# Optimization experiments

Measured on AMD Instinct MI355X. Metric: run time of the kernel, lower is better.

## Reference

```python
import jax, jax.numpy as jnp
import numpy as np

B, N, C, M = 2, 16384, 256, 16  # M = win_w*win_h for stage 1
W = N // M

def setup_inputs() -> dict:
    key = jax.random.key(0)
    ks = jax.random.split(key, 8)
    s = 1.0 / np.sqrt(C)
    return {
        "input": jax.random.normal(ks[0], (B, N, C), jnp.float32),
        "embed_qk": jax.random.normal(ks[1], (B, W, M, M, 3), jnp.float32),
        "Wq": jax.random.normal(ks[2], (C, C), jnp.float32) * s,
        "bq": jax.random.normal(ks[3], (C,), jnp.float32) * 0.01,
        "Wk": jax.random.normal(ks[4], (C, C), jnp.float32) * s,
        "bk": jax.random.normal(ks[5], (C,), jnp.float32) * 0.01,
        "Wp": jax.random.normal(ks[6], (3, 1), jnp.float32) * 0.5,
        "bp": jax.random.normal(ks[7], (1,), jnp.float32) * 0.01,
    }

def reference(input, embed_qk, Wq, bq, Wk, bk, Wp, bp):
    WIN = 16  # stage==1 -> win_w*win_h = 4*4
    b, n, c = input.shape
    add = (-n) % WIN
    q = jax.nn.elu(input @ Wq + bq) + 1.0
    k = jax.nn.elu(input @ Wk + bk) + 1.0
    v = input
    pad = ((0, 0), (0, add), (0, 0))
    q_win = jnp.pad(q, pad).reshape(b, -1, WIN, c)
    k_win = jnp.pad(k, pad).reshape(b, -1, WIN, c)
    v_win = jnp.pad(v, pad).reshape(b, -1, WIN, c)
    # second ELU+1 feature map (as in the original)
    phi_q = jax.nn.elu(q_win) + 1.0
    phi_k = jax.nn.elu(k_win) + 1.0
    # KV sums over ALL windows w -> (b, m, c, d)
    KV = jnp.einsum('bwmc,bwmd->bmcd', phi_k, v_win)
    # (b, w, n, m, d) expanded intermediate
    att = jnp.einsum('bwnc,bmcd->bwnmd', phi_q, KV)
    p = (embed_qk @ Wp + bp)[..., 0]  # (b, w, m, m)
    att = att + p[..., None]
    out = att.reshape(b, -1, c)[:, :n, :]
    return out
```

## Files before the change

kernel.cpp:

```cpp
#include <hip/hip_runtime.h>

typedef __attribute__((ext_vector_type(8))) short s16x8;
typedef __attribute__((ext_vector_type(8))) ushort u16x8;
typedef __attribute__((ext_vector_type(4))) ushort u16x4;
typedef __attribute__((ext_vector_type(4))) float f32x4v;

namespace {

constexpr int kB = 2;
constexpr int kN = 16384;
constexpr int kC = 256;
constexpr int kQR = 1024;

__device__ __forceinline__ ushort f2bf(float f) {
  union { float f; uint u; } v; v.f = f;
  uint u = v.u + 0x7fffu + ((v.u >> 16) & 1u);
  return (ushort)(u >> 16);
}

__device__ __forceinline__ float phi_act(float x) {
  return x > 0.f ? x + 2.f : __expf(x) + 1.f;
}

__global__ __launch_bounds__(256) void wt_kernel(const float* __restrict__ Wq,
                                                 const float* __restrict__ Wk,
                                                 ushort* __restrict__ WqT,
                                                 ushort* __restrict__ WkT) {
  __shared__ float ts[64][65];
  const float* W = blockIdx.z ? Wk : Wq;
  ushort* WT = blockIdx.z ? WkT : WqT;
  const int bi = blockIdx.x, bj = blockIdx.y, t = threadIdx.x;
  for (int rep = 0; rep < 16; ++rep) {
    int e = rep * 256 + t, r = e >> 6, c = e & 63;
    ts[r][c] = W[(size_t)(bi * 64 + r) * kC + bj * 64 + c];
  }
  __syncthreads();
  for (int rep = 0; rep < 16; ++rep) {
    int e = rep * 256 + t, j = e >> 6, k = e & 63;
    WT[(size_t)(bj * 64 + j) * kC + bi * 64 + k] = f2bf(ts[k][j]);
  }
}

__global__ __launch_bounds__(256) void regroup_kernel(const float* __restrict__ X,
                                                      ushort* __restrict__ G) {
  __shared__ ushort ls[64 * 288];
  const int cb = blockIdx.x;
  const int wb = blockIdx.y;
  const int b = blockIdx.z;
  const int t = threadIdx.x;
  const float* src = X + ((size_t)b * kN + wb * 1024) * kC + cb * 16;
  const int lr = t >> 2, cg = t & 3;
  for (int rep = 0; rep < 16; ++rep) {
    int row = rep * 64 + lr;
    float4 v = *reinterpret_cast<const float4*>(src + (size_t)row * kC + cg * 4);
    int w = row >> 4, m = row & 15;
    int base = w * 288 + m * 18 + cg * 4;
    uint p0 = (uint)f2bf(v.x) | ((uint)f2bf(v.y) << 16);
    uint p1 = (uint)f2bf(v.z) | ((uint)f2bf(v.w) << 16);
    *reinterpret_cast<uint*>(ls + base) = p0;
    *reinterpret_cast<uint*>(ls + base + 2) = p1;
  }
  __syncthreads();
  const int m = t >> 4, c_l = t & 15;
  const size_t gbase = ((size_t)b * 16 + m) * 128 + wb * 8;
#pragma unroll
  for (int r = 0; r < 8; ++r) {
    u16x8 v;
#pragma unroll
    for (int wl = 0; wl < 8; ++wl) v[wl] = ls[(r * 8 + wl) * 288 + m * 18 + c_l];
    *reinterpret_cast<u16x8*>(G + (gbase + r) * 2048 + (size_t)(cb * 16 + c_l) * 8) = v;
  }
}

__global__ __launch_bounds__(512) void proj_fused(
    const float* __restrict__ X, const ushort* __restrict__ WqT,
    const ushort* __restrict__ WkT, const float* __restrict__ bq,
    const float* __restrict__ bk, ushort* __restrict__ kg,
    ushort* __restrict__ qf) {
  __shared__ __align__(16) ushort smem[24576];

  const int t = threadIdx.x, lane = t & 63, wv = t >> 6;
  const int bx = blockIdx.x;
  const bool kmode = bx < 256;
  int b, n0;
  const ushort* WT;
  const float* bias;
  if (kmode) {
    b = bx >> 7; n0 = (bx & 127) * 128; WT = WkT; bias = bk;
  } else {
    int i = bx - 256; b = i >> 3; n0 = (i & 7) * 128; WT = WqT; bias = bq;
  }
  const int wgrp = bx & 127;
  const float* Xbase = X + ((size_t)b * kN + n0) * kC;

  const int r4 = t >> 2, ca = (t & 3) << 3;
  const int bj = t >> 2, bch = t & 3;

  float4 fa0, fa1;
  u16x8 rb0, rb1;
  auto stageLoad = [&](int ks) {
    const int k0 = ks * 32;
    fa0 = *reinterpret_cast<const float4*>(Xbase + (size_t)r4 * kC + k0 + ca);
    fa1 = *reinterpret_cast<const float4*>(Xbase + (size_t)r4 * kC + k0 + ca + 4);
    rb0 = *reinterpret_cast<const u16x8*>(WT + (size_t)bj * kC + k0 + bch * 8);
    rb1 = *reinterpret_cast<const u16x8*>(WT + (size_t)(bj + 128) * kC + k0 + bch * 8);
  };
  auto stageWrite = [&](int h) {
    ushort* A = smem + h * 4096;
    ushort* B = smem + 8192 + h * 8192;
    u16x8 va;
    va[0] = f2bf(fa0.x); va[1] = f2bf(fa0.y); va[2] = f2bf(fa0.z); va[3] = f2bf(fa0.w);
    va[4] = f2bf(fa1.x); va[5] = f2bf(fa1.y); va[6] = f2bf(fa1.z); va[7] = f2bf(fa1.w);
    *reinterpret_cast<u16x8*>(A + r4 * 32 + (((t & 3) ^ ((r4 >> 1) & 3)) << 3)) = va;
    *reinterpret_cast<u16x8*>(B + bj * 32 + ((bch ^ ((bj >> 1) & 3)) << 3)) = rb0;
    *reinterpret_cast<u16x8*>(B + (bj + 128) * 32 + ((bch ^ (((bj + 128) >> 1) & 3)) << 3)) = rb1;
  };

  f32x4v acc[4][4] = {};
  const int lo = lane & 15, hi = lane >> 4;
  const int wr0 = (wv >> 2) * 64, wc0 = (wv & 3) * 64;
  auto mma = [&](int h) {
    const ushort* A = smem + h * 4096;
    const ushort* B = smem + 8192 + h * 8192;
    s16x8 af[4], bf[4];
#pragma unroll
    for (int i = 0; i < 4; ++i) {
      int r = wr0 + i * 16 + lo;
      af[i] = *reinterpret_cast<const s16x8*>(A + r * 32 + ((hi ^ ((r >> 1) & 3)) << 3));
    }
#pragma unroll
    for (int j = 0; j < 4; ++j) {
      int cj = wc0 + j * 16 + lo;
      bf[j] = *reinterpret_cast<const s16x8*>(B + cj * 32 + ((hi ^ ((cj >> 1) & 3)) << 3));
    }
#pragma unroll
    for (int i = 0; i < 4; ++i)
#pragma unroll
      for (int j = 0; j < 4; ++j)
        acc[i][j] = __builtin_amdgcn_mfma_f32_16x16x32_bf16(af[i], bf[j], acc[i][j], 0, 0, 0);
  };

  stageLoad(0);
  stageWrite(0);
  __syncthreads();
  int cur = 0;
  for (int ks = 0; ks < 8; ++ks) {
    if (ks < 7) stageLoad(ks + 1);
    __builtin_amdgcn_sched_barrier(0);
    mma(cur);
    __builtin_amdgcn_sched_barrier(0);
    if (ks < 7) stageWrite(cur ^ 1);
    __syncthreads();
    cur ^= 1;
  }

  float bv[4];
#pragma unroll
  for (int fj = 0; fj < 4; ++fj) bv[fj] = bias[wc0 + fj * 16 + lo];

  if (kmode) {
    const int m = t >> 5, cl = t & 31;
    u16x8 vout[8];
    ushort* ep = smem;
#pragma unroll
    for (int h = 0; h < 2; ++h) {
      __syncthreads();
      if ((wv >> 2) == h) {
#pragma unroll
        for (int fi = 0; fi < 4; ++fi)
#pragma unroll
          for (int fj = 0; fj < 4; ++fj)
#pragma unroll
            for (int r = 0; r < 4; ++r) {
              int rl = fi * 16 + hi * 4 + r;
              int col = wc0 + fj * 16 + lo;
              ep[rl * 260 + col] = f2bf(phi_act(acc[fi][fj][r] + bv[fj]));
            }
      }
      __syncthreads();
#pragma unroll
      for (int j = 0; j < 8; ++j) {
        int c = j * 32 + cl;
#pragma unroll
        for (int wl = 0; wl < 4; ++wl)
          vout[j][h * 4 + wl] = ep[(wl * 16 + m) * 260 + c];
      }
    }
#pragma unroll
    for (int j = 0; j < 8; ++j) {
      int c = j * 32 + cl;
      *reinterpret_cast<u16x8*>(
          kg + (((size_t)(b * 16 + m) * 128 + wgrp) * 256 + c) * 8) = vout[j];
    }
  } else {
#pragma unroll
    for (int fi = 0; fi < 4; ++fi)
#pragma unroll
      for (int fj = 0; fj < 4; ++fj)
#pragma unroll
        for (int r = 0; r < 4; ++r) {
          int row = n0 + wr0 + fi * 16 + hi * 4 + r;
          int col = wc0 + fj * 16 + lo;
          qf[((size_t)b * kQR + row) * kC + col] = f2bf(phi_act(acc[fi][fj][r] + bv[fj]));
        }
  }
}

__global__ __launch_bounds__(256) void kv_kernel(const ushort* __restrict__ kg,
                                                 const ushort* __restrict__ xg,
                                                 ushort* __restrict__ kvt) {
  __shared__ __align__(16) ushort smem[16384];
  const int t = threadIdx.x, lane = t & 63, wv = t >> 6;
  const int swz = (blockIdx.x & 7) * 64 + (blockIdx.x >> 3);
  const int bm = swz >> 4, cb = swz & 3, db = (swz >> 2) & 3;
  const int lc = t & 63, g2 = t >> 6;

  u16x8 ra0, ra1, rb0, rb1;
  auto stageLoad = [&](int ws) {
    size_t base = (size_t)bm * 128 + ws * 8;
    ra0 = *reinterpret_cast<const u16x8*>(kg + ((base + g2) * 256 + cb * 64 + lc) * 8);
    ra1 = *reinterpret_cast<const u16x8*>(kg + ((base + g2 + 4) * 256 + cb * 64 + lc) * 8);
    rb0 = *reinterpret_cast<const u16x8*>(xg + ((base + g2) * 256 + db * 64 + lc) * 8);
    rb1 = *reinterpret_cast<const u16x8*>(xg + ((base + g2 + 4) * 256 + db * 64 + lc) * 8);
  };
  auto stageWrite = [&](int h) {
    ushort* A = smem + h * 4096;
    ushort* B = smem + 8192 + h * 4096;
    int s = (lc >> 1) & 7;
    *reinterpret_cast<u16x8*>(A + lc * 64 + ((g2 ^ s) << 3)) = ra0;
    *reinterpret_cast<u16x8*>(A + lc * 64 + (((g2 + 4) ^ s) << 3)) = ra1;
    *reinterpret_cast<u16x8*>(B + lc * 64 + ((g2 ^ s) << 3)) = rb0;
    *reinterpret_cast<u16x8*>(B + lc * 64 + (((g2 + 4) ^ s) << 3)) = rb1;
  };

  f32x4v acc[2][2] = {};
  const int lo = lane & 15, hi = lane >> 4;
  const int wr0 = (wv >> 1) * 32, wc0 = (wv & 1) * 32;
  auto mma = [&](int h) {
    const ushort* A = smem + h * 4096;
    const ushort* B = smem + 8192 + h * 4096;
    s16x8 af[2][2], bf[2][2];
#pragma unroll
    for (int i = 0; i < 2; ++i) {
      int r = wr0 + i * 16 + lo;
      int s = (r >> 1) & 7;
#pragma unroll
      for (int kk = 0; kk < 2; ++kk)
        af[i][kk] = *reinterpret_cast<const s16x8*>(A + r * 64 + (((kk * 4 + hi) ^ s) << 3));
    }
#pragma unroll
    for (int j = 0; j < 2; ++j) {
      int c = wc0 + j * 16 + lo;
      int s = (c >> 1) & 7;
#pragma unroll
      for (int kk = 0; kk < 2; ++kk)
        bf[j][kk] = *reinterpret_cast<const s16x8*>(B + c * 64 + (((kk * 4 + hi) ^ s) << 3));
    }
#pragma unroll
    for (int kk = 0; kk < 2; ++kk)
#pragma unroll
      for (int i = 0; i < 2; ++i)
#pragma unroll
        for (int j = 0; j < 2; ++j)
          acc[i][j] = __builtin_amdgcn_mfma_f32_16x16x32_bf16(af[i][kk], bf[j][kk], acc[i][j], 0, 0, 0);
  };

  stageLoad(0);
  stageWrite(0);
  __syncthreads();
  int cur = 0;
  for (int ws = 0; ws < 16; ++ws) {
    if (ws < 15) stageLoad(ws + 1);
    __builtin_amdgcn_sched_barrier(0);
    mma(cur);
    __builtin_amdgcn_sched_barrier(0);
    if (ws < 15) stageWrite(cur ^ 1);
    __syncthreads();
    cur ^= 1;
  }
#pragma unroll
  for (int i = 0; i < 2; ++i)
#pragma unroll
    for (int j = 0; j < 2; ++j) {
      int d = db * 64 + wc0 + j * 16 + lo;
      int c = cb * 64 + wr0 + i * 16 + hi * 4;
      u16x4 v = {f2bf(acc[i][j][0]), f2bf(acc[i][j][1]), f2bf(acc[i][j][2]),
                 f2bf(acc[i][j][3])};
      *reinterpret_cast<u16x4*>(kvt + ((size_t)bm * 256 + d) * 256 + c) = v;
    }
}

__global__ __launch_bounds__(256) void out_kernel(
    const ushort* __restrict__ qf, const ushort* __restrict__ kvt,
    const float* __restrict__ EQK, const float* __restrict__ Wp,
    const float* __restrict__ bp, float* __restrict__ Out) {
  __shared__ __align__(16) ushort smem[16384];
  __shared__ float Ps[128];
  const int t = threadIdx.x, lane = t & 63, wv = t >> 6;
  const int swz = (blockIdx.x & 7) * 64 + (blockIdx.x >> 3);
  const int bm = swz >> 4, qb = swz & 7, db = (swz >> 3) & 1;
  const int b = bm >> 4, mm = bm & 15;
  if (t < 128) {
    int qr = qb * 128 + t;
    const float* e = EQK + (((size_t)(b * 1024 + (qr >> 4)) * 16 + (qr & 15)) * 16 + mm) * 3;
    Ps[t] = e[0] * Wp[0] + e[1] * Wp[1] + e[2] * Wp[2] + bp[0];
  }
  const int r2 = t >> 2, ch = t & 3;

  u16x8 ra0, ra1, rb0, rb1;
  auto stageLoad = [&](int ks) {
    int k0 = ks * 32;
    const ushort* Aq = qf + ((size_t)b * kQR + qb * 128) * kC;
    const ushort* Bk = kvt + ((size_t)bm * 256 + db * 128) * kC;
    ra0 = *reinterpret_cast<const u16x8*>(Aq + (size_t)r2 * kC + k0 + ch * 8);
    ra1 = *reinterpret_cast<const u16x8*>(Aq + (size_t)(r2 + 64) * kC + k0 + ch * 8);
    rb0 = *reinterpret_cast<const u16x8*>(Bk + (size_t)r2 * kC + k0 + ch * 8);
    rb1 = *reinterpret_cast<const u16x8*>(Bk + (size_t)(r2 + 64) * kC + k0 + ch * 8);
  };
  auto stageWrite = [&](int h) {
    ushort* A = smem + h * 4096;
    ushort* B = smem + 8192 + h * 4096;
    *reinterpret_cast<u16x8*>(A + r2 * 32 + ((ch ^ ((r2 >> 1) & 3)) << 3)) = ra0;
    *reinterpret_cast<u16x8*>(A + (r2 + 64) * 32 + ((ch ^ (((r2 + 64) >> 1) & 3)) << 3)) = ra1;
    *reinterpret_cast<u16x8*>(B + r2 * 32 + ((ch ^ ((r2 >> 1) & 3)) << 3)) = rb0;
    *reinterpret_cast<u16x8*>(B + (r2 + 64) * 32 + ((ch ^ (((r2 + 64) >> 1) & 3)) << 3)) = rb1;
  };

  f32x4v acc[4][4] = {};
  const int lo = lane & 15, hi = lane >> 4;
  const int wr0 = (wv >> 1) * 64, wc0 = (wv & 1) * 64;
  auto mma = [&](int h) {
    const ushort* A = smem + h * 4096;
    const ushort* B = smem + 8192 + h * 4096;
    s16x8 af[4], bf[4];
#pragma unroll
    for (int i = 0; i < 4; ++i) {
      int r = wr0 + i * 16 + lo;
      af[i] = *reinterpret_cast<const s16x8*>(A + r * 32 + ((hi ^ ((r >> 1) & 3)) << 3));
    }
#pragma unroll
    for (int j = 0; j < 4; ++j) {
      int c = wc0 + j * 16 + lo;
      bf[j] = *reinterpret_cast<const s16x8*>(B + c * 32 + ((hi ^ ((c >> 1) & 3)) << 3));
    }
#pragma unroll
    for (int i = 0; i < 4; ++i)
#pragma unroll
      for (int j = 0; j < 4; ++j)
        acc[i][j] = __builtin_amdgcn_mfma_f32_16x16x32_bf16(af[i], bf[j], acc[i][j], 0, 0, 0);
  };

  stageLoad(0);
  stageWrite(0);
  __syncthreads();
  int cur = 0;
  for (int ks = 0; ks < 8; ++ks) {
    if (ks < 7) stageLoad(ks + 1);
    __builtin_amdgcn_sched_barrier(0);
    mma(cur);
    __builtin_amdgcn_sched_barrier(0);
    if (ks < 7) stageWrite(cur ^ 1);
    __syncthreads();
    cur ^= 1;
  }
#pragma unroll
  for (int fi = 0; fi < 4; ++fi)
#pragma unroll
    for (int r4 = 0; r4 < 4; ++r4) {
      int rowl = wr0 + fi * 16 + hi * 4 + r4;
      int qr = qb * 128 + rowl;
      float p = Ps[rowl];
      size_t orow = ((size_t)b * kN + (size_t)qr * 16 + mm) * kC;
#pragma unroll
      for (int fj = 0; fj < 4; ++fj) {
        int d = db * 128 + wc0 + fj * 16 + lo;
        Out[orow + d] = acc[fi][fj][r4] + p;
      }
    }
}

}

extern "C" void kernel_launch(void* const* d_in, const int* in_sizes, int n_in,
                              void* d_out, int out_size, void* d_ws,
                              size_t ws_size, hipStream_t stream) {
  const float* input = (const float*)d_in[0];
  const float* eqk = (const float*)d_in[1];
  const float* Wq = (const float*)d_in[2];
  const float* bq = (const float*)d_in[3];
  const float* Wk = (const float*)d_in[4];
  const float* bk = (const float*)d_in[5];
  const float* Wp = (const float*)d_in[6];
  const float* bp = (const float*)d_in[7];
  float* out = (float*)d_out;

  ushort* ws = (ushort*)d_ws;
  ushort* WqT = ws;
  ushort* WkT = WqT + 65536;
  ushort* xg = WkT + 65536;
  ushort* kg = xg + 8388608;
  ushort* qf = kg + 8388608;
  ushort* kvt = qf + 524288;

  wt_kernel<<<dim3(4, 4, 2), 256, 0, stream>>>(Wq, Wk, WqT, WkT);
  regroup_kernel<<<dim3(16, 16, 2), 256, 0, stream>>>(input, xg);
  proj_fused<<<dim3(272), 512, 0, stream>>>(input, WqT, WkT, bq, bk, kg, qf);
  kv_kernel<<<dim3(512), 256, 0, stream>>>(kg, xg, kvt);
  out_kernel<<<dim3(512), 256, 0, stream>>>(qf, kvt, eqk, Wp, bp, out);
}
```

Measured before the change: 145.9 us.

## Retile projection, regroup and KV kernels for more blocks and deeper K steps

The projection kernel moves from 272 blocks of 512 threads with 128x256 tiles to 1088 blocks of 256 threads with 64x128 tiles. It keeps the full 128x256 weight slice resident in swizzled shared memory and streams only the activations. The regroup kernel uses 4x more, smaller blocks, and the KV kernel doubles its K-chunk per stage so it runs half as many synchronized iterations. The aim is better occupancy and fewer barriers, at the cost of reloading weights per block and more LDS per block.

```diff
diff --git a/kernel.cpp b/kernel.cpp
--- a/kernel.cpp
+++ b/kernel.cpp
@@ -43,14 +43,15 @@
 
 __global__ __launch_bounds__(256) void regroup_kernel(const float* __restrict__ X,
                                                       ushort* __restrict__ G) {
-  __shared__ ushort ls[64 * 288];
+  __shared__ ushort ls[16 * 288];
   const int cb = blockIdx.x;
   const int wb = blockIdx.y;
   const int b = blockIdx.z;
   const int t = threadIdx.x;
-  const float* src = X + ((size_t)b * kN + wb * 1024) * kC + cb * 16;
+  const float* src = X + ((size_t)b * kN + wb * 256) * kC + cb * 16;
   const int lr = t >> 2, cg = t & 3;
-  for (int rep = 0; rep < 16; ++rep) {
+#pragma unroll
+  for (int rep = 0; rep < 4; ++rep) {
     int row = rep * 64 + lr;
     float4 v = *reinterpret_cast<const float4*>(src + (size_t)row * kC + cg * 4);
     int w = row >> 4, m = row & 15;
@@ -62,146 +63,140 @@
   }
   __syncthreads();
   const int m = t >> 4, c_l = t & 15;
-  const size_t gbase = ((size_t)b * 16 + m) * 128 + wb * 8;
-#pragma unroll
-  for (int r = 0; r < 8; ++r) {
+#pragma unroll
+  for (int oct = 0; oct < 2; ++oct) {
     u16x8 v;
 #pragma unroll
-    for (int wl = 0; wl < 8; ++wl) v[wl] = ls[(r * 8 + wl) * 288 + m * 18 + c_l];
-    *reinterpret_cast<u16x8*>(G + (gbase + r) * 2048 + (size_t)(cb * 16 + c_l) * 8) = v;
-  }
-}
-
-__global__ __launch_bounds__(512) void proj_fused(
+    for (int wl = 0; wl < 8; ++wl) v[wl] = ls[(oct * 8 + wl) * 288 + m * 18 + c_l];
+    *reinterpret_cast<u16x8*>(
+        G + (((size_t)(b * 16 + m) * 128 + wb * 2 + oct) * 256 + cb * 16 + c_l) * 8) = v;
+  }
+}
+
+__global__ __launch_bounds__(256) void proj_kernel(
     const float* __restrict__ X, const ushort* __restrict__ WqT,
     const ushort* __restrict__ WkT, const float* __restrict__ bq,
     const float* __restrict__ bk, ushort* __restrict__ kg,
     ushort* __restrict__ qf) {
-  __shared__ __align__(16) ushort smem[24576];
+  __shared__ __align__(16) ushort smem[36864];
 
   const int t = threadIdx.x, lane = t & 63, wv = t >> 6;
   const int bx = blockIdx.x;
-  const bool kmode = bx < 256;
-  int b, n0;
+  const bool kmode = bx < 1024;
+  int b, n0, jb;
   const ushort* WT;
   const float* bias;
   if (kmode) {
-    b = bx >> 7; n0 = (bx & 127) * 128; WT = WkT; bias = bk;
+    b = bx >> 9; int rem = bx & 511; n0 = (rem >> 1) * 64; jb = bx & 1;
+    WT = WkT; bias = bk;
   } else {
-    int i = bx - 256; b = i >> 3; n0 = (i & 7) * 128; WT = WqT; bias = bq;
-  }
-  const int wgrp = bx & 127;
-  const float* Xbase = X + ((size_t)b * kN + n0) * kC;
-
-  const int r4 = t >> 2, ca = (t & 3) << 3;
-  const int bj = t >> 2, bch = t & 3;
-
+    int i = bx - 1024; b = i >> 5; int rem = i & 31; n0 = (rem >> 1) * 64; jb = i & 1;
+    WT = WqT; bias = bq;
+  }
+  const int j0 = jb * 128;
+  const float* Xb = X + ((size_t)b * kN + n0) * kC;
+
+  for (int rep = 0; rep < 16; ++rep) {
+    int idx = rep * 256 + t;
+    int jj = idx >> 5, cc = idx & 31;
+    u16x8 v = *reinterpret_cast<const u16x8*>(WT + (size_t)(j0 + jj) * kC + cc * 8);
+    *reinterpret_cast<u16x8*>(smem + jj * 256 + ((cc ^ (jj & 31)) << 3)) = v;
+  }
+
+  const int aq = t & 7, ar = t >> 3;
   float4 fa0, fa1;
-  u16x8 rb0, rb1;
-  auto stageLoad = [&](int ks) {
-    const int k0 = ks * 32;
-    fa0 = *reinterpret_cast<const float4*>(Xbase + (size_t)r4 * kC + k0 + ca);
-    fa1 = *reinterpret_cast<const float4*>(Xbase + (size_t)r4 * kC + k0 + ca + 4);
-    rb0 = *reinterpret_cast<const u16x8*>(WT + (size_t)bj * kC + k0 + bch * 8);
-    rb1 = *reinterpret_cast<const u16x8*>(WT + (size_t)(bj + 128) * kC + k0 + bch * 8);
-  };
-  auto stageWrite = [&](int h) {
-    ushort* A = smem + h * 4096;
-    ushort* B = smem + 8192 + h * 8192;
-    u16x8 va;
-    va[0] = f2bf(fa0.x); va[1] = f2bf(fa0.y); va[2] = f2bf(fa0.z); va[3] = f2bf(fa0.w);
-    va[4] = f2bf(fa1.x); va[5] = f2bf(fa1.y); va[6] = f2bf(fa1.z); va[7] = f2bf(fa1.w);
-    *reinterpret_cast<u16x8*>(A + r4 * 32 + (((t & 3) ^ ((r4 >> 1) & 3)) << 3)) = va;
-    *reinterpret_cast<u16x8*>(B + bj * 32 + ((bch ^ ((bj >> 1) & 3)) << 3)) = rb0;
-    *reinterpret_cast<u16x8*>(B + (bj + 128) * 32 + ((bch ^ (((bj + 128) >> 1) & 3)) << 3)) = rb1;
-  };
-
-  f32x4v acc[4][4] = {};
+  auto aLoad = [&](int s) {
+    fa0 = *reinterpret_cast<const float4*>(Xb + (size_t)ar * kC + s * 32 + aq * 4);
+    fa1 = *reinterpret_cast<const float4*>(Xb + (size_t)(ar + 32) * kC + s * 32 + aq * 4);
+  };
+  auto aWrite = [&](int h) {
+    ushort* A = smem + 32768 + h * 2048;
+    u16x4 v0 = {f2bf(fa0.x), f2bf(fa0.y), f2bf(fa0.z), f2bf(fa0.w)};
+    u16x4 v1 = {f2bf(fa1.x), f2bf(fa1.y), f2bf(fa1.z), f2bf(fa1.w)};
+    *reinterpret_cast<u16x4*>(A + ar * 32 + (((aq >> 1) ^ ((ar >> 1) & 3)) << 3) +
+                              (aq & 1) * 4) = v0;
+    const int r1 = ar + 32;
+    *reinterpret_cast<u16x4*>(A + r1 * 32 + (((aq >> 1) ^ ((r1 >> 1) & 3)) << 3) +
+                              (aq & 1) * 4) = v1;
+  };
+
   const int lo = lane & 15, hi = lane >> 4;
-  const int wr0 = (wv >> 2) * 64, wc0 = (wv & 3) * 64;
-  auto mma = [&](int h) {
-    const ushort* A = smem + h * 4096;
-    const ushort* B = smem + 8192 + h * 8192;
-    s16x8 af[4], bf[4];
-#pragma unroll
-    for (int i = 0; i < 4; ++i) {
+  const int wr0 = (wv >> 1) * 32, wc0 = (wv & 1) * 64;
+  f32x4v acc[2][4] = {};
+  auto mma = [&](int h, int s) {
+    const ushort* A = smem + 32768 + h * 2048;
+    s16x8 a[2], bf[4];
+#pragma unroll
+    for (int i = 0; i < 2; ++i) {
       int r = wr0 + i * 16 + lo;
-      af[i] = *reinterpret_cast<const s16x8*>(A + r * 32 + ((hi ^ ((r >> 1) & 3)) << 3));
-    }
-#pragma unroll
-    for (int j = 0; j < 4; ++j) {
-      int cj = wc0 + j * 16 + lo;
-      bf[j] = *reinterpret_cast<const s16x8*>(B + cj * 32 + ((hi ^ ((cj >> 1) & 3)) << 3));
-    }
-#pragma unroll
-    for (int i = 0; i < 4; ++i)
-#pragma unroll
-      for (int j = 0; j < 4; ++j)
-        acc[i][j] = __builtin_amdgcn_mfma_f32_16x16x32_bf16(af[i], bf[j], acc[i][j], 0, 0, 0);
-  };
-
-  stageLoad(0);
-  stageWrite(0);
+      a[i] = *reinterpret_cast<const s16x8*>(A + r * 32 + ((hi ^ ((r >> 1) & 3)) << 3));
+    }
+#pragma unroll
+    for (int fj = 0; fj < 4; ++fj) {
+      int j = wc0 + fj * 16 + lo;
+      bf[fj] = *reinterpret_cast<const s16x8*>(
+          smem + j * 256 + (((s * 4 + hi) ^ (j & 31)) << 3));
+    }
+#pragma unroll
+    for (int i = 0; i < 2; ++i)
+#pragma unroll
+      for (int fj = 0; fj < 4; ++fj)
+        acc[i][fj] = __builtin_amdgcn_mfma_f32_16x16x32_bf16(a[i], bf[fj], acc[i][fj], 0, 0, 0);
+  };
+
+  aLoad(0);
+  aWrite(0);
   __syncthreads();
   int cur = 0;
-  for (int ks = 0; ks < 8; ++ks) {
-    if (ks < 7) stageLoad(ks + 1);
-    __builtin_amdgcn_sched_barrier(0);
-    mma(cur);
-    __builtin_amdgcn_sched_barrier(0);
-    if (ks < 7) stageWrite(cur ^ 1);
+  for (int s = 0; s < 8; ++s) {
+    if (s < 7) aLoad(s + 1);
+    __builtin_amdgcn_sched_barrier(0);
+    mma(cur, s);
+    __builtin_amdgcn_sched_barrier(0);
+    if (s < 7) aWrite(cur ^ 1);
     __syncthreads();
     cur ^= 1;
   }
 
   float bv[4];
 #pragma unroll
-  for (int fj = 0; fj < 4; ++fj) bv[fj] = bias[wc0 + fj * 16 + lo];
+  for (int fj = 0; fj < 4; ++fj) bv[fj] = bias[j0 + wc0 + fj * 16 + lo];
 
   if (kmode) {
-    const int m = t >> 5, cl = t & 31;
-    u16x8 vout[8];
+    __syncthreads();
     ushort* ep = smem;
 #pragma unroll
-    for (int h = 0; h < 2; ++h) {
-      __syncthreads();
-      if ((wv >> 2) == h) {
-#pragma unroll
-        for (int fi = 0; fi < 4; ++fi)
-#pragma unroll
-          for (int fj = 0; fj < 4; ++fj)
-#pragma unroll
-            for (int r = 0; r < 4; ++r) {
-              int rl = fi * 16 + hi * 4 + r;
-              int col = wc0 + fj * 16 + lo;
-              ep[rl * 260 + col] = f2bf(phi_act(acc[fi][fj][r] + bv[fj]));
-            }
-      }
-      __syncthreads();
-#pragma unroll
-      for (int j = 0; j < 8; ++j) {
-        int c = j * 32 + cl;
-#pragma unroll
-        for (int wl = 0; wl < 4; ++wl)
-          vout[j][h * 4 + wl] = ep[(wl * 16 + m) * 260 + c];
-      }
-    }
-#pragma unroll
-    for (int j = 0; j < 8; ++j) {
-      int c = j * 32 + cl;
-      *reinterpret_cast<u16x8*>(
-          kg + (((size_t)(b * 16 + m) * 128 + wgrp) * 256 + c) * 8) = vout[j];
+    for (int i = 0; i < 2; ++i)
+#pragma unroll
+      for (int fj = 0; fj < 4; ++fj)
+#pragma unroll
+        for (int r = 0; r < 4; ++r) {
+          int row = wr0 + i * 16 + hi * 4 + r;
+          int col = wc0 + fj * 16 + lo;
+          ep[row * 128 + col] = f2bf(phi_act(acc[i][fj][r] + bv[fj]));
+        }
+    __syncthreads();
+    const int m = t >> 4, cl = t & 15;
+    const int wgrp = n0 >> 7, sub = (n0 >> 6) & 1;
+#pragma unroll
+    for (int rep = 0; rep < 8; ++rep) {
+      int c = rep * 16 + cl;
+      u16x4 v;
+#pragma unroll
+      for (int wl = 0; wl < 4; ++wl) v[wl] = ep[(wl * 16 + m) * 128 + c];
+      *reinterpret_cast<u16x4*>(
+          kg + (((size_t)(b * 16 + m) * 128 + wgrp) * 256 + j0 + c) * 8 + sub * 4) = v;
     }
   } else {
 #pragma unroll
-    for (int fi = 0; fi < 4; ++fi)
+    for (int i = 0; i < 2; ++i)
 #pragma unroll
       for (int fj = 0; fj < 4; ++fj)
 #pragma unroll
         for (int r = 0; r < 4; ++r) {
-          int row = n0 + wr0 + fi * 16 + hi * 4 + r;
-          int col = wc0 + fj * 16 + lo;
-          qf[((size_t)b * kQR + row) * kC + col] = f2bf(phi_act(acc[fi][fj][r] + bv[fj]));
+          int row = n0 + wr0 + i * 16 + hi * 4 + r;
+          int col = j0 + wc0 + fj * 16 + lo;
+          qf[((size_t)b * kQR + row) * kC + col] = f2bf(phi_act(acc[i][fj][r] + bv[fj]));
         }
   }
 }
@@ -209,83 +204,86 @@
 __global__ __launch_bounds__(256) void kv_kernel(const ushort* __restrict__ kg,
                                                  const ushort* __restrict__ xg,
                                                  ushort* __restrict__ kvt) {
-  __shared__ __align__(16) ushort smem[16384];
+  __shared__ __align__(16) ushort smem[32768];
   const int t = threadIdx.x, lane = t & 63, wv = t >> 6;
   const int swz = (blockIdx.x & 7) * 64 + (blockIdx.x >> 3);
   const int bm = swz >> 4, cb = swz & 3, db = (swz >> 2) & 3;
-  const int lc = t & 63, g2 = t >> 6;
-
-  u16x8 ra0, ra1, rb0, rb1;
-  auto stageLoad = [&](int ws) {
-    size_t base = (size_t)bm * 128 + ws * 8;
-    ra0 = *reinterpret_cast<const u16x8*>(kg + ((base + g2) * 256 + cb * 64 + lc) * 8);
-    ra1 = *reinterpret_cast<const u16x8*>(kg + ((base + g2 + 4) * 256 + cb * 64 + lc) * 8);
-    rb0 = *reinterpret_cast<const u16x8*>(xg + ((base + g2) * 256 + db * 64 + lc) * 8);
-    rb1 = *reinterpret_cast<const u16x8*>(xg + ((base + g2 + 4) * 256 + db * 64 + lc) * 8);
-  };
-  auto stageWrite = [&](int h) {
-    ushort* A = smem + h * 4096;
-    ushort* B = smem + 8192 + h * 4096;
-    int s = (lc >> 1) & 7;
-    *reinterpret_cast<u16x8*>(A + lc * 64 + ((g2 ^ s) << 3)) = ra0;
-    *reinterpret_cast<u16x8*>(A + lc * 64 + (((g2 + 4) ^ s) << 3)) = ra1;
-    *reinterpret_cast<u16x8*>(B + lc * 64 + ((g2 ^ s) << 3)) = rb0;
-    *reinterpret_cast<u16x8*>(B + lc * 64 + (((g2 + 4) ^ s) << 3)) = rb1;
-  };
-
-  f32x4v acc[2][2] = {};
+  const int lc = t & 63, g = t >> 6;
+  const ushort* Ab = kg + (size_t)bm * 262144 + (size_t)(cb * 64 + lc) * 8;
+  const ushort* Bb = xg + (size_t)bm * 262144 + (size_t)(db * 64 + lc) * 8;
+
+  u16x8 ra[4], rb[4];
+  auto sLoad = [&](int s) {
+#pragma unroll
+    for (int q = 0; q < 4; ++q) {
+      const size_t w8 = (size_t)(s * 16 + g + q * 4) * 2048;
+      ra[q] = *reinterpret_cast<const u16x8*>(Ab + w8);
+      rb[q] = *reinterpret_cast<const u16x8*>(Bb + w8);
+    }
+  };
+  auto sWrite = [&](int h) {
+    ushort* A = smem + h * 8192;
+    ushort* B = smem + 16384 + h * 8192;
+    const int fl = (lc & 15) ^ (lc >> 4);
+#pragma unroll
+    for (int q = 0; q < 4; ++q) {
+      int o = g + q * 4;
+      *reinterpret_cast<u16x8*>(A + lc * 128 + ((o ^ fl) << 3)) = ra[q];
+      *reinterpret_cast<u16x8*>(B + lc * 128 + ((o ^ fl) << 3)) = rb[q];
+    }
+  };
+
   const int lo = lane & 15, hi = lane >> 4;
   const int wr0 = (wv >> 1) * 32, wc0 = (wv & 1) * 32;
+  f32x4v acc[2][2] = {};
   auto mma = [&](int h) {
-    const ushort* A = smem + h * 4096;
-    const ushort* B = smem + 8192 + h * 4096;
-    s16x8 af[2][2], bf[2][2];
-#pragma unroll
-    for (int i = 0; i < 2; ++i) {
-      int r = wr0 + i * 16 + lo;
-      int s = (r >> 1) & 7;
-#pragma unroll
-      for (int kk = 0; kk < 2; ++kk)
-        af[i][kk] = *reinterpret_cast<const s16x8*>(A + r * 64 + (((kk * 4 + hi) ^ s) << 3));
-    }
-#pragma unroll
-    for (int j = 0; j < 2; ++j) {
-      int c = wc0 + j * 16 + lo;
-      int s = (c >> 1) & 7;
-#pragma unroll
-      for (int kk = 0; kk < 2; ++kk)
-        bf[j][kk] = *reinterpret_cast<const s16x8*>(B + c * 64 + (((kk * 4 + hi) ^ s) << 3));
-    }
-#pragma unroll
-    for (int kk = 0; kk < 2; ++kk)
-#pragma unroll
-      for (int i = 0; i < 2; ++i)
-#pragma unroll
-        for (int j = 0; j < 2; ++j)
-          acc[i][j] = __builtin_amdgcn_mfma_f32_16x16x32_bf16(af[i][kk], bf[j][kk], acc[i][j], 0, 0, 0);
-  };
-
-  stageLoad(0);
-  stageWrite(0);
+    const ushort* A = smem + h * 8192;
+    const ushort* B = smem + 16384 + h * 8192;
+#pragma unroll
+    for (int kk = 0; kk < 4; ++kk) {
+      s16x8 a0, a1, b0, b1;
+      {
+        int r = wr0 + lo;
+        a0 = *reinterpret_cast<const s16x8*>(
+            A + r * 128 + (((kk * 4 + hi) ^ ((r & 15) ^ (r >> 4))) << 3));
+        int r2 = wr0 + 16 + lo;
+        a1 = *reinterpret_cast<const s16x8*>(
+            A + r2 * 128 + (((kk * 4 + hi) ^ ((r2 & 15) ^ (r2 >> 4))) << 3));
+        int c = wc0 + lo;
+        b0 = *reinterpret_cast<const s16x8*>(
+            B + c * 128 + (((kk * 4 + hi) ^ ((c & 15) ^ (c >> 4))) << 3));
+        int c2 = wc0 + 16 + lo;
+        b1 = *reinterpret_cast<const s16x8*>(
+            B + c2 * 128 + (((kk * 4 + hi) ^ ((c2 & 15) ^ (c2 >> 4))) << 3));
+      }
+      acc[0][0] = __builtin_amdgcn_mfma_f32_16x16x32_bf16(a0, b0, acc[0][0], 0, 0, 0);
+      acc[0][1] = __builtin_amdgcn_mfma_f32_16x16x32_bf16(a0, b1, acc[0][1], 0, 0, 0);
+      acc[1][0] = __builtin_amdgcn_mfma_f32_16x16x32_bf16(a1, b0, acc[1][0], 0, 0, 0);
+      acc[1][1] = __builtin_amdgcn_mfma_f32_16x16x32_bf16(a1, b1, acc[1][1], 0, 0, 0);
+    }
+  };
+
+  sLoad(0);
+  sWrite(0);
   __syncthreads();
   int cur = 0;
-  for (int ws = 0; ws < 16; ++ws) {
-    if (ws < 15) stageLoad(ws + 1);
+  for (int s = 0; s < 8; ++s) {
+    if (s < 7) sLoad(s + 1);
     __builtin_amdgcn_sched_barrier(0);
     mma(cur);
     __builtin_amdgcn_sched_barrier(0);
-    if (ws < 15) stageWrite(cur ^ 1);
+    if (s < 7) sWrite(cur ^ 1);
     __syncthreads();
     cur ^= 1;
   }
 #pragma unroll
-  for (int i = 0; i < 2; ++i)
-#pragma unroll
-    for (int j = 0; j < 2; ++j) {
-      int d = db * 64 + wc0 + j * 16 + lo;
-      int c = cb * 64 + wr0 + i * 16 + hi * 4;
-      u16x4 v = {f2bf(acc[i][j][0]), f2bf(acc[i][j][1]), f2bf(acc[i][j][2]),
-                 f2bf(acc[i][j][3])};
+  for (int fi = 0; fi < 2; ++fi)
+#pragma unroll
+    for (int fj = 0; fj < 2; ++fj) {
+      int d = db * 64 + wc0 + fj * 16 + lo;
+      int c = cb * 64 + wr0 + fi * 16 + hi * 4;
+      u16x4 v = {f2bf(acc[fi][fj][0]), f2bf(acc[fi][fj][1]),
+                 f2bf(acc[fi][fj][2]), f2bf(acc[fi][fj][3])};
       *reinterpret_cast<u16x4*>(kvt + ((size_t)bm * 256 + d) * 256 + c) = v;
     }
 }
@@ -403,8 +401,8 @@
   ushort* kvt = qf + 524288;
 
   wt_kernel<<<dim3(4, 4, 2), 256, 0, stream>>>(Wq, Wk, WqT, WkT);
-  regroup_kernel<<<dim3(16, 16, 2), 256, 0, stream>>>(input, xg);
-  proj_fused<<<dim3(272), 512, 0, stream>>>(input, WqT, WkT, bq, bk, kg, qf);
+  regroup_kernel<<<dim3(16, 64, 2), 256, 0, stream>>>(input, xg);
+  proj_kernel<<<dim3(1088), 256, 0, stream>>>(input, WqT, WkT, bq, bk, kg, qf);
   kv_kernel<<<dim3(512), 256, 0, stream>>>(kg, xg, kvt);
   out_kernel<<<dim3(512), 256, 0, stream>>>(qf, kvt, eqk, Wp, bp, out);
 }
```

After: 154.4 us. 5.9% more time.
